# Optimization experiments

Measured on AMD Instinct MI355X. Metric: run time of the kernel, lower is better.

The kernel has to match this reference:

```python
import jax, jax.numpy as jnp
from jax import lax
import numpy as np

B, P, G, C = 16, 6000, 128, 10
PC_MIN = np.array([-54.0, -54.0, -5.0], np.float32)
PC_MAX = np.array([54.0, 54.0, 3.0], np.float32)
CENTER_RADIUS = 1.5
CANDIDATE_TOPK = 5
NUM_HEADS = 6
CLS_W, ALPHA, GAMMA = 2.0, 0.25, 2.0
REG_W, IOU_W = 0.25, 0.25
EPS = 1e-12
INF1, INF2 = 10000.0, 100000.0


def _aabb(boxes):
    # boxes: (N,7) [cx,cy,cz,dx,dy,dz,yaw] -> AABB (min,max) of the 8 rotated corners
    c, d, yaw = boxes[:, :3], boxes[:, 3:6], boxes[:, 6]
    ca, sa = jnp.abs(jnp.cos(yaw)), jnp.abs(jnp.sin(yaw))
    hx = 0.5 * (d[:, 0] * ca + d[:, 1] * sa)
    hy = 0.5 * (d[:, 0] * sa + d[:, 1] * ca)
    h = jnp.stack([hx, hy, 0.5 * d[:, 2]], -1)
    return c - h, c + h


def _iou3d(pred7, gt7):
    # axis-aligned 3D IoU over corner AABBs (reference stand-in for rotated BboxOverlaps3D)
    pmin, pmax = _aabb(pred7)
    gmin, gmax = _aabb(gt7)
    lo = jnp.maximum(pmin[:, None], gmin[None])   # (P,G,3)
    hi = jnp.minimum(pmax[:, None], gmax[None])
    inter = jnp.prod(jnp.maximum(hi - lo, 0.0), -1)
    vp = jnp.prod(pmax - pmin, -1)
    vg = jnp.prod(gmax - gmin, -1)
    return inter / (vp[:, None] + vg[None] - inter + 1e-7)


def _cost_matrix(pred_logits, pred_boxes, gt_boxes, gt_labels):
    # --- focal classification cost ---
    p = jax.nn.sigmoid(pred_logits)                                  # (P,C)
    neg = -jnp.log(1.0 - p + EPS) * (1.0 - ALPHA) * p ** GAMMA
    pos = -jnp.log(p + EPS) * ALPHA * (1.0 - p) ** GAMMA
    cls_cost = (pos - neg)[:, gt_labels] * CLS_W                     # (P,G)

    gt_norm = jnp.concatenate([gt_boxes[:, :3], jnp.log(gt_boxes[:, 3:6]),
                               jnp.sin(gt_boxes[:, 6:7]), jnp.cos(gt_boxes[:, 6:7])], -1)  # (G,8)
    reg_cost = jnp.abs(pred_boxes[:, None, :8] - gt_norm[None]).sum(-1) * REG_W

    # --- IoU cost on denormalized pred boxes ---
    yaw = jnp.arctan2(pred_boxes[:, 6], pred_boxes[:, 7])
    pred7 = jnp.concatenate([pred_boxes[:, :3], jnp.exp(pred_boxes[:, 3:6]), yaw[:, None]], -1)
    ious = _iou3d(pred7, gt_boxes)                                   # (P,G)
    iou_cost = -ious * IOU_W

    # --- in-gt-box / in-center geometric prior ---
    ctr = pred_boxes[:, :3]
    gmin, gmax = _aabb(gt_boxes)
    in_box = jnp.all((ctr[:, None] > gmin[None]) & (ctr[:, None] < gmax[None]), -1)  # (P,G)
    gc, gd = gt_boxes[:, :3], gt_boxes[:, 3:6]
    lo = gc - CENTER_RADIUS * gd
    hi = gc + CENTER_RADIUS * gd
    in_ctr = jnp.all((ctr[:, None] > lo[None]) & (ctr[:, None] < hi[None]), -1)
    valid = jnp.any(in_box, 1) | jnp.any(in_ctr, 1)                  # (P,)
    in_both = in_box & in_ctr

    cost = cls_cost + reg_cost + iou_cost + (~in_both).astype(cls_cost.dtype) * 100.0
    cost = cost + (~valid).astype(cls_cost.dtype)[:, None] * INF1
    return cost, ious, valid


def _assign(pred_logits, pred_boxes, gt_boxes, gt_labels, head_idx):
    cost, ious, valid = _cost_matrix(pred_logits, pred_boxes, gt_boxes, gt_labels)

    # dynamic-k per gt: sum of top-k ious minus head-schedule offset, truncated, min 1
    k = min(CANDIDATE_TOPK, P)
    topk_ious = lax.top_k(ious.T, k)[0]                              # (G,k)
    dyn = jnp.maximum((topk_ious.sum(1) - 0.5 * (NUM_HEADS - head_idx)).astype(jnp.int32), 1)

    # per-gt lowest-cost top-dyn selection via double argsort ranks
    ranks = jnp.argsort(jnp.argsort(cost, axis=0), axis=0)           # (P,G)
    matching = (ranks < dyn[None, :]).astype(cost.dtype)

    # priors matched to >1 gt: keep only the min-cost gt
    prior_mask = matching.sum(1) > 1
    onehot_min = jax.nn.one_hot(jnp.argmin(cost, 1), G, dtype=cost.dtype)
    matching = jnp.where(prior_mask[:, None], onehot_min, matching)

    rows = jnp.arange(P)

    def cond(s):
        i, cst, m = s
        return jnp.any(m.sum(0) == 0) & (i < G + 8)

    def body(s):
        i, cst, m = s
        cst = cst + (m.sum(1) > 0).astype(cst.dtype)[:, None] * INF2
        unmatched = m.sum(0) == 0                                    # (G,)
        pos = jnp.argmin(cst, 0)                                     # (G,) best prior per gt
        m = jnp.where((rows[:, None] == pos[None]) & unmatched[None], 1.0, m)
        over = jnp.any(m.sum(1) > 1)
        oh = jax.nn.one_hot(jnp.argmin(cst, 1), G, dtype=cst.dtype)
        m = jnp.where(over & prior_mask[:, None], oh, m)             # stale mask, as in torch source
        return i + 1, cst, m

    _, _, matching = lax.while_loop(cond, body, (jnp.int32(0), cost, matching))

    fg = matching.sum(1) > 0                                         # (P,) foreground mask
    matched = jnp.where(fg, jnp.argmax(matching, 1), -1).astype(jnp.int32)
    return fg, matched


def setup_inputs():
    key = jax.random.key(0)
    k1, k2, k3, k4, k5, k6, k7, k8 = jax.random.split(key, 8)
    pred_logits = jax.random.normal(k1, (B, P, C), jnp.float32)
    ctr = jax.random.uniform(k2, (B, P, 3), jnp.float32, jnp.array(PC_MIN), jnp.array(PC_MAX))
    logsz = jnp.log(jax.random.uniform(k3, (B, P, 3), jnp.float32, 1.0, 4.0))
    ang = jax.random.uniform(k4, (B, P, 1), jnp.float32, -np.pi, np.pi)
    vel = jax.random.normal(k5, (B, P, 2), jnp.float32)
    pred_boxes = jnp.concatenate([ctr, logsz, jnp.sin(ang), jnp.cos(ang), vel], -1)
    gctr = jax.random.uniform(k6, (B, G, 3), jnp.float32, jnp.array(PC_MIN), jnp.array(PC_MAX))
    gsz = jax.random.uniform(k7, (B, G, 3), jnp.float32, 1.0, 5.0)
    gyaw = jax.random.uniform(k8, (B, G, 1), jnp.float32, -np.pi, np.pi)
    gt_boxes = jnp.concatenate([gctr, gsz, gyaw], -1)
    gt_labels = jax.random.randint(jax.random.fold_in(key, 99), (B, G), 0, C)
    return {"pred_logits": pred_logits, "pred_boxes": pred_boxes,
            "gt_boxes": gt_boxes, "gt_labels": gt_labels, "head_idx": 5}


def reference(pred_logits, pred_boxes, gt_boxes, gt_labels, head_idx):
    f = lambda pl, pb, gb, gl: _assign(pl, pb, gb, gl, head_idx)
    fg, matched = jax.vmap(f)(pred_logits, pred_boxes, gt_boxes, gt_labels)
    return fg, matched
```

## Files before the change

kernel.cpp:

```cpp
#include <hip/hip_runtime.h>
#include <stdint.h>
#include <math.h>

#define NB 16
#define NP 6000
#define NG 128
#define NC 10
#define SELMAX 4
#define GSTR 24
#define CPB 2
#define PS 2
#define PPC 3000
#define QS 12
#define EPIW 128

typedef unsigned long long u64;
#define NBPs ((size_t)NB * NP)

__device__ __forceinline__ uint32_t fkey(float f) {
  uint32_t u = __float_as_uint(f);
  return (u & 0x80000000u) ? ~u : (u | 0x80000000u);
}
__device__ __forceinline__ float fkey_inv(uint32_t k) {
  uint32_t u = (k & 0x80000000u) ? (k & 0x7fffffffu) : ~k;
  return __uint_as_float(u);
}
__device__ __forceinline__ u64 shfl_xor_u64(u64 v, int m) {
  uint32_t lo = (uint32_t)v, hi = (uint32_t)(v >> 32);
  lo = (uint32_t)__shfl_xor((int)lo, m, 64);
  hi = (uint32_t)__shfl_xor((int)hi, m, 64);
  return ((u64)hi << 32) | lo;
}
__device__ __forceinline__ u64 block_min_u64(u64 v, u64* sred, int lane, int wid) {
  for (int o = 1; o < 64; o <<= 1) {
    u64 t = shfl_xor_u64(v, o);
    if (t < v) v = t;
  }
  __syncthreads();
  if (lane == 0) sred[wid] = v;
  __syncthreads();
  u64 r = sred[0];
  if (sred[1] < r) r = sred[1];
  if (sred[2] < r) r = sred[2];
  if (sred[3] < r) r = sred[3];
  return r;
}

__device__ __forceinline__ void ins5max(uint32_t& a0, uint32_t& a1, uint32_t& a2,
                                        uint32_t& a3, uint32_t& a4, uint32_t k) {
  if (k > a4) {
    a4 = k;
    if (a4 > a3) { uint32_t t = a4; a4 = a3; a3 = t; }
    if (a3 > a2) { uint32_t t = a3; a3 = a2; a2 = t; }
    if (a2 > a1) { uint32_t t = a2; a2 = a1; a1 = t; }
    if (a1 > a0) { uint32_t t = a1; a1 = a0; a0 = t; }
  }
}
__device__ __forceinline__ void ins4min(u64& c0, u64& c1, u64& c2, u64& c3, u64 k) {
  if (k < c3) {
    c3 = k;
    if (c3 < c2) { u64 t = c3; c3 = c2; c2 = t; }
    if (c2 < c1) { u64 t = c2; c2 = c1; c1 = t; }
    if (c1 < c0) { u64 t = c1; c1 = c0; c0 = t; }
  }
}
__device__ __forceinline__ void wave_top5_iou(uint32_t a0, uint32_t a1,
                                              uint32_t a2, uint32_t a3,
                                              uint32_t a4, int lane,
                                              float* dst) {
  int hp = 0;
  for (int k = 0; k < 5; ++k) {
    uint32_t cand = (hp == 0) ? a0 : (hp == 1) ? a1 : (hp == 2) ? a2
                  : (hp == 3) ? a3 : (hp == 4) ? a4 : 0u;
    u64 key = ((u64)cand << 32) | (unsigned)lane;
    u64 r = key;
    for (int o = 1; o < 64; o <<= 1) {
      u64 t = shfl_xor_u64(r, o);
      if (t > r) r = t;
    }
    if (lane == 0) dst[k] = fkey_inv((uint32_t)(r >> 32));
    if (r == key) hp++;
  }
}
__device__ __forceinline__ void wave_top4_cost(u64 c0, u64 c1, u64 c2, u64 c3,
                                               int lane, u64* dst) {
  int hp = 0;
  for (int k = 0; k < 4; ++k) {
    u64 cand = (hp == 0) ? c0 : (hp == 1) ? c1 : (hp == 2) ? c2
             : (hp == 3) ? c3 : ~0ull;
    u64 r = cand;
    for (int o = 1; o < 64; o <<= 1) {
      u64 t = shfl_xor_u64(r, o);
      if (t < r) r = t;
    }
    if (lane == 0) dst[k] = r;
    if (r == cand) hp++;
  }
}

__global__ __launch_bounds__(256) void prep_kernel(
    const float* __restrict__ gt_boxes,
    const int* __restrict__ gt_labels,
    const float* __restrict__ pred_logits,
    const float* __restrict__ pred_boxes,
    float* __restrict__ gtaux,
    float* __restrict__ paux,
    float* __restrict__ clst,
    int* __restrict__ rowcnt,
    int* __restrict__ rowassign,
    int* __restrict__ colcnt,
    int* __restrict__ wcount) {
#pragma clang fp contract(off)
  __shared__ float shg[NG * 12];
  const int b = blockIdx.y, tid = threadIdx.x;
  if (tid < NG) {
    const int g = tid;
    const float* gb = gt_boxes + ((size_t)b * NG + g) * 7;
    float cx = gb[0], cy = gb[1], cz = gb[2];
    float dx = gb[3], dy = gb[4], dz = gb[5];
    float yaw = gb[6];
    float cyw = cosf(yaw), syw = sinf(yaw);
    float ca = fabsf(cyw), sa = fabsf(syw);
    float hx = 0.5f * (dx * ca + dy * sa);
    float hy = 0.5f * (dx * sa + dy * ca);
    float hz = 0.5f * dz;
    float gmin0 = cx - hx, gmin1 = cy - hy, gmin2 = cz - hz;
    float gmax0 = cx + hx, gmax1 = cy + hy, gmax2 = cz + hz;
    float* s = &shg[g * 12];
    s[0] = gmin0; s[1] = gmin1; s[2] = gmin2;
    s[3] = gmax0; s[4] = gmax1; s[5] = gmax2;
    s[6] = cx - 1.5f * dx; s[7] = cy - 1.5f * dy; s[8] = cz - 1.5f * dz;
    s[9] = cx + 1.5f * dx; s[10] = cy + 1.5f * dy; s[11] = cz + 1.5f * dz;
    if (blockIdx.x == 0) {
      float vg = ((gmax0 - gmin0) * (gmax1 - gmin1)) * (gmax2 - gmin2);
      float* o = gtaux + ((size_t)b * NG + g) * GSTR;
      o[0] = gmin0; o[1] = gmin1; o[2] = gmin2;
      o[3] = gmax0; o[4] = gmax1; o[5] = gmax2;
      o[6] = s[6]; o[7] = s[7]; o[8] = s[8];
      o[9] = s[9]; o[10] = s[10]; o[11] = s[11];
      o[12] = cx; o[13] = cy; o[14] = cz;
      o[15] = logf(dx); o[16] = logf(dy); o[17] = logf(dz);
      o[18] = syw; o[19] = cyw;
      o[20] = vg;
      o[21] = __int_as_float(gt_labels[(size_t)b * NG + g]);
      o[22] = 0.0f; o[23] = 0.0f;
      colcnt[b * NG + g] = 0;
      if (b == 0 && g == 0) wcount[0] = 0;
    }
  }
  __syncthreads();
  const int p = blockIdx.x * 256 + tid;
  if (p >= NP) return;
  const size_t idx = (size_t)b * NP + p;
  const float* lg = pred_logits + idx * NC;
  for (int c = 0; c < NC; ++c) {
    float x = lg[c];
    float pr = 1.0f / (1.0f + expf(-x));
    float neg = (-logf(1.0f - pr + 1e-12f) * 0.75f) * (pr * pr);
    float pos = (-logf(pr + 1e-12f) * 0.25f) * ((1.0f - pr) * (1.0f - pr));
    clst[(size_t)c * NBPs + idx] = (pos - neg) * 2.0f;
  }
  const float* bx = pred_boxes + idx * 10;
  float b0 = bx[0], b1 = bx[1], b2 = bx[2], b3 = bx[3], b4 = bx[4];
  float b5 = bx[5], b6 = bx[6], b7 = bx[7];
  float yaw = atan2f(b6, b7);
  float d0 = expf(b3), d1 = expf(b4), d2 = expf(b5);
  float ca = fabsf(cosf(yaw)), sa = fabsf(sinf(yaw));
  float hx = 0.5f * (d0 * ca + d1 * sa);
  float hy = 0.5f * (d0 * sa + d1 * ca);
  float hz = 0.5f * d2;
  float pmin0 = b0 - hx, pmin1 = b1 - hy, pmin2 = b2 - hz;
  float pmax0 = b0 + hx, pmax1 = b1 + hy, pmax2 = b2 + hz;
  int valid = 0;
  for (int g = 0; g < NG; ++g) {
    const float* s = &shg[g * 12];
    bool inb = (b0 > s[0]) && (b0 < s[3]) && (b1 > s[1]) && (b1 < s[4]) &&
               (b2 > s[2]) && (b2 < s[5]);
    bool inc = (b0 > s[6]) && (b0 < s[9]) && (b1 > s[7]) && (b1 < s[10]) &&
               (b2 > s[8]) && (b2 < s[11]);
    if (inb || inc) { valid = 1; break; }
  }
  float* o = paux + idx * 16;
  o[0] = b0; o[1] = b1; o[2] = b2; o[3] = b3;
  o[4] = b4; o[5] = b5; o[6] = b6; o[7] = b7;
  o[8] = pmin0; o[9] = pmin1; o[10] = pmin2;
  o[11] = pmax0; o[12] = pmax1; o[13] = pmax2;
  o[14] = ((pmax0 - pmin0) * (pmax1 - pmin1)) * (pmax2 - pmin2);
  o[15] = valid ? 0.0f : 10000.0f;
  rowcnt[idx] = 0;
  rowassign[idx] = 0x7fffffff;
}

struct GTp {
  float gmin0, gmin1, gmin2, gmax0, gmax1, gmax2;
  float lo0, lo1, lo2, hi0, hi1, hi2;
  float gtn0, gtn1, gtn2, gtn3, gtn4, gtn5, gtn6, gtn7;
  float vg;
  int label;
};
__device__ __forceinline__ GTp load_gt(const float* __restrict__ gtaux,
                                       int b, int g) {
  const float* ga = gtaux + ((size_t)b * NG + g) * GSTR;
  GTp t;
  t.gmin0 = ga[0]; t.gmin1 = ga[1]; t.gmin2 = ga[2];
  t.gmax0 = ga[3]; t.gmax1 = ga[4]; t.gmax2 = ga[5];
  t.lo0 = ga[6]; t.lo1 = ga[7]; t.lo2 = ga[8];
  t.hi0 = ga[9]; t.hi1 = ga[10]; t.hi2 = ga[11];
  t.gtn0 = ga[12]; t.gtn1 = ga[13]; t.gtn2 = ga[14]; t.gtn3 = ga[15];
  t.gtn4 = ga[16]; t.gtn5 = ga[17]; t.gtn6 = ga[18]; t.gtn7 = ga[19];
  t.vg = ga[20];
  t.label = __float_as_int(ga[21]);
  return t;
}

__device__ __forceinline__ float cost_base(
    float b0, float b1, float b2, float b3, float b4, float b5, float b6,
    float b7, float pmin0, float pmin1, float pmin2, float pmax0, float pmax1,
    float pmax2, float vp, float cls, const GTp& t, float* iou_out) {
#pragma clang fp contract(off)
  float r = fabsf(b0 - t.gtn0);
  r = r + fabsf(b1 - t.gtn1);
  r = r + fabsf(b2 - t.gtn2);
  r = r + fabsf(b3 - t.gtn3);
  r = r + fabsf(b4 - t.gtn4);
  r = r + fabsf(b5 - t.gtn5);
  r = r + fabsf(b6 - t.gtn6);
  r = r + fabsf(b7 - t.gtn7);
  float reg = r * 0.25f;
  float li0 = fmaxf(pmin0, t.gmin0), li1 = fmaxf(pmin1, t.gmin1),
        li2 = fmaxf(pmin2, t.gmin2);
  float hj0 = fminf(pmax0, t.gmax0), hj1 = fminf(pmax1, t.gmax1),
        hj2 = fminf(pmax2, t.gmax2);
  float e0 = fmaxf(hj0 - li0, 0.0f), e1 = fmaxf(hj1 - li1, 0.0f),
        e2 = fmaxf(hj2 - li2, 0.0f);
  float inter = (e0 * e1) * e2;
  float iou = inter / (((vp + t.vg) - inter) + 1e-7f);
  bool inb = (b0 > t.gmin0) && (b0 < t.gmax0) && (b1 > t.gmin1) &&
             (b1 < t.gmax1) && (b2 > t.gmin2) && (b2 < t.gmax2);
  bool inc = (b0 > t.lo0) && (b0 < t.hi0) && (b1 > t.lo1) && (b1 < t.hi1) &&
             (b2 > t.lo2) && (b2 < t.hi2);
  *iou_out = iou;
  return ((cls + reg) + (-(iou * 0.25f))) + ((inb && inc) ? 0.0f : 100.0f);
}

__device__ __forceinline__ void eval_fast(
    float b0, float b1, float b2, float b3, float b4, float b5, float b6,
    float b7, float pmin0, float pmin1, float pmin2, float pmax0, float pmax1,
    float pmax2, float vp, float cls, const GTp& t,
    uint32_t& a0, uint32_t& a1, uint32_t& a2, uint32_t& a3, uint32_t& a4,
    float* cc_out) {
#pragma clang fp contract(off)
  float r = fabsf(b0 - t.gtn0);
  r = r + fabsf(b1 - t.gtn1);
  r = r + fabsf(b2 - t.gtn2);
  r = r + fabsf(b3 - t.gtn3);
  r = r + fabsf(b4 - t.gtn4);
  r = r + fabsf(b5 - t.gtn5);
  r = r + fabsf(b6 - t.gtn6);
  r = r + fabsf(b7 - t.gtn7);
  float reg = r * 0.25f;
  bool ov = (pmin0 < t.gmax0) && (pmax0 > t.gmin0) &&
            (pmin1 < t.gmax1) && (pmax1 > t.gmin1) &&
            (pmin2 < t.gmax2) && (pmax2 > t.gmin2);
  float cc;
  if (ov) {
    float li0 = fmaxf(pmin0, t.gmin0), li1 = fmaxf(pmin1, t.gmin1),
          li2 = fmaxf(pmin2, t.gmin2);
    float hj0 = fminf(pmax0, t.gmax0), hj1 = fminf(pmax1, t.gmax1),
          hj2 = fminf(pmax2, t.gmax2);
    float e0 = fmaxf(hj0 - li0, 0.0f), e1 = fmaxf(hj1 - li1, 0.0f),
          e2 = fmaxf(hj2 - li2, 0.0f);
    float inter = (e0 * e1) * e2;
    float iou = inter / (((vp + t.vg) - inter) + 1e-7f);
    bool inb = (b0 > t.gmin0) && (b0 < t.gmax0) && (b1 > t.gmin1) &&
               (b1 < t.gmax1) && (b2 > t.gmin2) && (b2 < t.gmax2);
    bool inc = (b0 > t.lo0) && (b0 < t.hi0) && (b1 > t.lo1) && (b1 < t.hi1) &&
               (b2 > t.lo2) && (b2 < t.hi2);
    cc = ((cls + reg) + (-(iou * 0.25f))) + ((inb && inc) ? 0.0f : 100.0f);
    ins5max(a0, a1, a2, a3, a4, fkey(iou));
  } else {
    cc = (cls + reg) + 100.0f;
  }
  *cc_out = cc;
}

__global__ __launch_bounds__(256) void select_kernel(
    const float* __restrict__ paux,
    const float* __restrict__ clst,
    const float* __restrict__ gtaux,
    float* __restrict__ iou5F,
    u64* __restrict__ ckF) {
#pragma clang fp contract(off)
  const int n = blockIdx.x;
  const int orig = (n & 7) * 256 + (n >> 3);
  const int b = orig >> 7;
  const int rem = orig & 127;
  const int gq = rem >> 1, ps = rem & 1;
  const int g0 = gq * CPB;
  const int tid = threadIdx.x;
  const int lane = tid & 63, wid = tid >> 6;

  const GTp t0 = load_gt(gtaux, b, g0);
  const GTp t1 = load_gt(gtaux, b, g0 + 1);
  const size_t rowbase = (size_t)b * NP;
  const int pbase = ps * PPC;

  const uint32_t Z = fkey(0.0f);
  uint32_t i0a = Z, i0b = Z, i0c = Z, i0d = Z, i0e = Z;
  uint32_t i1a = Z, i1b = Z, i1c = Z, i1d = Z, i1e = Z;
  u64 k0a = ~0ull, k0b = ~0ull, k0c = ~0ull, k0d = ~0ull;
  u64 k1a = ~0ull, k1b = ~0ull, k1c = ~0ull, k1d = ~0ull;

  for (int q = 0; q < QS; ++q) {
    const int off = q * 256 + tid;
    if (off < PPC) {
      const int p = pbase + off;
      const size_t idx = rowbase + p;
      const float4* pa = (const float4*)(paux + idx * 16);
      float4 A = pa[0], B = pa[1], C = pa[2], D = pa[3];
      float cls0 = clst[(size_t)t0.label * NBPs + idx];
      float cls1 = clst[(size_t)t1.label * NBPs + idx];
      float cc0, cc1;
      eval_fast(A.x, A.y, A.z, A.w, B.x, B.y, B.z, B.w,
                C.x, C.y, C.z, C.w, D.x, D.y, D.z, cls0, t0,
                i0a, i0b, i0c, i0d, i0e, &cc0);
      eval_fast(A.x, A.y, A.z, A.w, B.x, B.y, B.z, B.w,
                C.x, C.y, C.z, C.w, D.x, D.y, D.z, cls1, t1,
                i1a, i1b, i1c, i1d, i1e, &cc1);
      ins4min(k0a, k0b, k0c, k0d, ((u64)fkey(cc0 + D.w) << 32) | (unsigned)p);
      ins4min(k1a, k1b, k1c, k1d, ((u64)fkey(cc1 + D.w) << 32) | (unsigned)p);
    }
  }

  __shared__ float iouW[4][CPB][5];
  __shared__ u64 ckW[4][CPB][4];
  wave_top5_iou(i0a, i0b, i0c, i0d, i0e, lane, &iouW[wid][0][0]);
  wave_top5_iou(i1a, i1b, i1c, i1d, i1e, lane, &iouW[wid][1][0]);
  wave_top4_cost(k0a, k0b, k0c, k0d, lane, &ckW[wid][0][0]);
  wave_top4_cost(k1a, k1b, k1c, k1d, lane, &ckW[wid][1][0]);
  __syncthreads();

  if (tid < CPB) {
    const int c = tid;
    const int col = b * NG + g0 + c;
    float m0 = -INFINITY, m1 = -INFINITY, m2 = -INFINITY, m3 = -INFINITY,
          m4 = -INFINITY;
    for (int w = 0; w < 4; ++w) {
      for (int j = 0; j < 5; ++j) {
        float v = iouW[w][c][j];
        if (v > m4) {
          m4 = v;
          if (m4 > m3) { float t = m4; m4 = m3; m3 = t; }
          if (m3 > m2) { float t = m3; m3 = m2; m2 = t; }
          if (m2 > m1) { float t = m2; m2 = m1; m1 = t; }
          if (m1 > m0) { float t = m1; m1 = m0; m0 = t; }
        }
      }
    }
    u64 s0 = ~0ull, s1 = ~0ull, s2 = ~0ull, s3 = ~0ull;
    for (int w = 0; w < 4; ++w) {
      for (int j = 0; j < 4; ++j) {
        u64 k = ckW[w][c][j];
        if (k < s3) {
          s3 = k;
          if (s3 < s2) { u64 t = s3; s3 = s2; s2 = t; }
          if (s2 < s1) { u64 t = s2; s2 = s1; s1 = t; }
          if (s1 < s0) { u64 t = s1; s1 = s0; s0 = t; }
        }
      }
    }
    float* fi = iou5F + (size_t)col * (PS * 5) + ps * 5;
    fi[0] = m0; fi[1] = m1; fi[2] = m2; fi[3] = m3; fi[4] = m4;
    u64* fc = ckF + (size_t)col * (PS * 4) + ps * 4;
    fc[0] = s0; fc[1] = s1; fc[2] = s2; fc[3] = s3;
  }
}

__global__ __launch_bounds__(256) void merge_kernel(
    const float* __restrict__ iou5F,
    const u64* __restrict__ ckF,
    const int* __restrict__ head_ptr,
    int* __restrict__ colsel,
    int* __restrict__ rowcnt,
    int* __restrict__ rowassign,
    int* __restrict__ wlist,
    int* __restrict__ wcount) {
#pragma clang fp contract(off)
  const int col = blockIdx.x * 256 + threadIdx.x;
  if (col >= NB * NG) return;
  const int b = col / NG, g = col - b * NG;
  const float* ip = iou5F + (size_t)col * (PS * 5);
  float m0 = -INFINITY, m1 = -INFINITY, m2 = -INFINITY, m3 = -INFINITY,
        m4 = -INFINITY;
  for (int i = 0; i < PS * 5; ++i) {
    float v = ip[i];
    if (v > m4) {
      m4 = v;
      if (m4 > m3) { float t = m4; m4 = m3; m3 = t; }
      if (m3 > m2) { float t = m3; m3 = m2; m2 = t; }
      if (m2 > m1) { float t = m2; m2 = m1; m1 = t; }
      if (m1 > m0) { float t = m1; m1 = m0; m0 = t; }
    }
  }
  float sum5 = ((((m0 + m1) + m2) + m3) + m4);
  float adj = sum5 - 0.5f * (float)(6 - head_ptr[0]);
  int dyn = (int)adj;
  if (dyn < 1) dyn = 1;
  if (dyn > SELMAX) dyn = SELMAX;

  const u64* kp = ckF + (size_t)col * (PS * 4);
  u64 s0 = ~0ull, s1 = ~0ull, s2 = ~0ull, s3 = ~0ull;
  for (int i = 0; i < PS * 4; ++i) {
    u64 k = kp[i];
    if (k < s3) {
      s3 = k;
      if (s3 < s2) { u64 t = s3; s3 = s2; s2 = t; }
      if (s2 < s1) { u64 t = s2; s2 = s1; s1 = t; }
      if (s1 < s0) { u64 t = s1; s1 = s0; s0 = t; }
    }
  }
  const size_t rowbase = (size_t)b * NP;
  int pk[4];
  pk[0] = (int)(s0 & 0xffffffffu);
  pk[1] = (int)(s1 & 0xffffffffu);
  pk[2] = (int)(s2 & 0xffffffffu);
  pk[3] = (int)(s3 & 0xffffffffu);
  for (int k = 0; k < SELMAX; ++k) {
    int sel = (k < dyn) ? pk[k] : -1;
    colsel[(size_t)col * SELMAX + k] = sel;
    if (sel >= 0) {
      int old = atomicAdd(&rowcnt[rowbase + sel], 1);
      if (old == 1) {
        int slot = atomicAdd(wcount, 1);
        wlist[slot] = (int)(rowbase + sel);
      }
      atomicMin(&rowassign[rowbase + sel], g);
    }
  }
}

__global__ __launch_bounds__(256) void epi_kernel(
    const float* __restrict__ paux,
    const float* __restrict__ clst,
    const float* __restrict__ gtaux,
    const int* __restrict__ colsel,
    const int* __restrict__ rowcnt,
    const int* __restrict__ wlist,
    const int* __restrict__ wcount,
    int* __restrict__ rowminArr,
    int* __restrict__ colcnt) {
#pragma clang fp contract(off)
  const int tid = threadIdx.x;
  if (blockIdx.x >= EPIW) {
    const int col = (blockIdx.x - EPIW) * 256 + tid;
    if (col < NB * NG) {
      const int b = col / NG;
      int cnt = 0;
      const size_t cb = (size_t)col * SELMAX;
      for (int k = 0; k < SELMAX; ++k) {
        int s = colsel[cb + k];
        if (s >= 0 && rowcnt[(size_t)b * NP + s] == 1) cnt++;
      }
      if (cnt) atomicAdd(&colcnt[col], cnt);
    }
    return;
  }
  const int lane = tid & 63, wid = tid >> 6;
  const int wavesTotal = EPIW * 4;
  const int wave = blockIdx.x * 4 + wid;
  const int n = wcount[0];
  for (int e = wave; e < n; e += wavesTotal) {
    const int idx = wlist[e];
    const int b = idx / NP;
    const float4* pa = (const float4*)(paux + (size_t)idx * 16);
    float4 A = pa[0], Bq = pa[1], Cq = pa[2], Dq = pa[3];
    const float pen = Dq.w;
    u64 best = ~0ull;
    for (int h = 0; h < 2; ++h) {
      const int g = h * 64 + lane;
      GTp t = load_gt(gtaux, b, g);
      float cls = clst[(size_t)t.label * NBPs + idx];
      float iou;
      float cc = cost_base(A.x, A.y, A.z, A.w, Bq.x, Bq.y, Bq.z, Bq.w,
                           Cq.x, Cq.y, Cq.z, Cq.w, Dq.x, Dq.y, Dq.z,
                           cls, t, &iou);
      u64 key = ((u64)fkey(cc + pen) << 32) | (unsigned)g;
      if (key < best) best = key;
    }
    for (int o = 1; o < 64; o <<= 1) {
      u64 t = shfl_xor_u64(best, o);
      if (t < best) best = t;
    }
    if (lane == 0) {
      const int bg = (int)(best & 0xffffffffu);
      rowminArr[idx] = bg;
      atomicAdd(&colcnt[b * NG + bg], 1);
    }
  }
}

__global__ __launch_bounds__(256) void fixup_kernel(
    const float* __restrict__ paux,
    const float* __restrict__ clst,
    const float* __restrict__ gtaux,
    const int* __restrict__ colcnt,
    const int* __restrict__ rowcnt,
    int* __restrict__ rowassign) {
#pragma clang fp contract(off)
  const int g = blockIdx.x, b = blockIdx.y, tid = threadIdx.x;
  if (colcnt[b * NG + g] != 0) return;
  const int lane = tid & 63, wid = tid >> 6;
  const size_t rowbase = (size_t)b * NP;
  GTp t = load_gt(gtaux, b, g);
  u64 best = ~0ull;
  for (int p = tid; p < NP; p += 256) {
    const size_t idx = rowbase + p;
    if (rowcnt[idx] == 0) {
      const float4* pa = (const float4*)(paux + idx * 16);
      float4 A = pa[0], Bq = pa[1], Cq = pa[2], Dq = pa[3];
      float cls = clst[(size_t)t.label * NBPs + idx];
      float iou;
      float cc = cost_base(A.x, A.y, A.z, A.w, Bq.x, Bq.y, Bq.z, Bq.w,
                           Cq.x, Cq.y, Cq.z, Cq.w, Dq.x, Dq.y, Dq.z,
                           cls, t, &iou);
      u64 key = ((u64)fkey(cc + Dq.w) << 32) | (unsigned)p;
      if (key < best) best = key;
    }
  }
  __shared__ u64 sred[4];
  u64 rr = block_min_u64(best, sred, lane, wid);
  if (tid == 0) {
    int pos = (int)(rr & 0xffffffffu);
    atomicMin(&rowassign[rowbase + pos], g);
  }
}

__global__ void output_kernel(const int* __restrict__ rowcnt,
                              const int* __restrict__ rowassign,
                              const int* __restrict__ rowminArr,
                              int* __restrict__ out) {
  const int i = blockIdx.x * 256 + threadIdx.x;
  if (i >= (int)NBPs) return;
  int rc = rowcnt[i];
  int fg, m;
  if (rc == 0) {
    int ra = rowassign[i];
    if (ra == 0x7fffffff) { fg = 0; m = -1; }
    else { fg = 1; m = ra; }
  } else if (rc == 1) {
    fg = 1; m = rowassign[i];
  } else {
    fg = 1; m = rowminArr[i];
  }
  out[i] = fg;
  out[NBPs + i] = m;
}

extern "C" void kernel_launch(void* const* d_in, const int* in_sizes, int n_in,
                              void* d_out, int out_size, void* d_ws, size_t ws_size,
                              hipStream_t stream) {
  const float* pred_logits = (const float*)d_in[0];
  const float* pred_boxes = (const float*)d_in[1];
  const float* gt_boxes = (const float*)d_in[2];
  const int* gt_labels = (const int*)d_in[3];
  const int* head = (const int*)d_in[4];
  (void)in_sizes; (void)n_in; (void)out_size; (void)ws_size;

  char* w = (char*)d_ws;
  size_t off = 0;
  auto alloc = [&](size_t bytes) -> void* {
    void* p = w + off;
    off += (bytes + 255) & ~(size_t)255;
    return p;
  };
  float* paux = (float*)alloc((size_t)NB * NP * 16 * 4);
  float* clst = (float*)alloc((size_t)NC * NB * NP * 4);
  float* gtaux = (float*)alloc((size_t)NB * NG * GSTR * 4);
  float* iou5F = (float*)alloc((size_t)NB * NG * PS * 5 * 4);
  u64* ckF = (u64*)alloc((size_t)NB * NG * PS * 4 * 8);
  int* colsel = (int*)alloc((size_t)NB * NG * SELMAX * 4);
  int* rowcnt = (int*)alloc((size_t)NB * NP * 4);
  int* rowassign = (int*)alloc((size_t)NB * NP * 4);
  int* rowminArr = (int*)alloc((size_t)NB * NP * 4);
  int* colcnt = (int*)alloc((size_t)NB * NG * 4);
  int* wlist = (int*)alloc((size_t)NB * NP * 4);
  int* wcount = (int*)alloc(256);

  int* out = (int*)d_out;
  dim3 blk(256);
  prep_kernel<<<dim3((NP + 255) / 256, NB), blk, 0, stream>>>(
      gt_boxes, gt_labels, pred_logits, pred_boxes, gtaux, paux, clst,
      rowcnt, rowassign, colcnt, wcount);
  select_kernel<<<dim3(NB * (NG / CPB) * PS), blk, 0, stream>>>(
      paux, clst, gtaux, iou5F, ckF);
  merge_kernel<<<dim3((NB * NG + 255) / 256), blk, 0, stream>>>(
      iou5F, ckF, head, colsel, rowcnt, rowassign, wlist, wcount);
  epi_kernel<<<dim3(EPIW + 8), blk, 0, stream>>>(
      paux, clst, gtaux, colsel, rowcnt, wlist, wcount, rowminArr, colcnt);
  fixup_kernel<<<dim3(NG, NB), blk, 0, stream>>>(
      paux, clst, gtaux, colcnt, rowcnt, rowassign);
  output_kernel<<<dim3(((int)NBPs + 255) / 256), blk, 0, stream>>>(
      rowcnt, rowassign, rowminArr, out);
}
```

Measured before the change: 118.6 us.

## Split prep validity scan across waves and process four GT columns per select block

```diff
diff --git a/kernel.cpp b/kernel.cpp
--- a/kernel.cpp
+++ b/kernel.cpp
@@ -8,10 +8,10 @@
 #define NC 10
 #define SELMAX 4
 #define GSTR 24
-#define CPB 2
-#define PS 2
-#define PPC 3000
-#define QS 12
+#define CPB 4
+#define PS 3
+#define PPC 2000
+#define QS 8
 #define EPIW 128
 
 typedef unsigned long long u64;
@@ -98,7 +98,7 @@
   }
 }
 
-__global__ __launch_bounds__(256) void prep_kernel(
+__global__ __launch_bounds__(512) void prep_kernel(
     const float* __restrict__ gt_boxes,
     const int* __restrict__ gt_labels,
     const float* __restrict__ pred_logits,
@@ -112,7 +112,9 @@
     int* __restrict__ wcount) {
 #pragma clang fp contract(off)
   __shared__ float shg[NG * 12];
+  __shared__ int vfl[8][64];
   const int b = blockIdx.y, tid = threadIdx.x;
+  const int lane = tid & 63, sub = tid >> 6;
   if (tid < NG) {
     const int g = tid;
     const float* gb = gt_boxes + ((size_t)b * NG + g) * 7;
@@ -149,46 +151,56 @@
     }
   }
   __syncthreads();
-  const int p = blockIdx.x * 256 + tid;
+  const int p = blockIdx.x * 64 + lane;
+  const size_t idx = (size_t)b * NP + p;
+  int flag = 0;
+  if (p < NP) {
+    const float* bxp = pred_boxes + idx * 10;
+    float b0 = bxp[0], b1 = bxp[1], b2 = bxp[2];
+    for (int g = sub * 16; g < sub * 16 + 16; ++g) {
+      const float* s = &shg[g * 12];
+      bool inb = (b0 > s[0]) && (b0 < s[3]) && (b1 > s[1]) && (b1 < s[4]) &&
+                 (b2 > s[2]) && (b2 < s[5]);
+      bool inc = (b0 > s[6]) && (b0 < s[9]) && (b1 > s[7]) && (b1 < s[10]) &&
+                 (b2 > s[8]) && (b2 < s[11]);
+      if (inb || inc) { flag = 1; break; }
+    }
+  }
+  vfl[sub][lane] = flag;
+  __syncthreads();
   if (p >= NP) return;
-  const size_t idx = (size_t)b * NP + p;
   const float* lg = pred_logits + idx * NC;
-  for (int c = 0; c < NC; ++c) {
+  for (int c = sub; c < NC; c += 8) {
     float x = lg[c];
     float pr = 1.0f / (1.0f + expf(-x));
     float neg = (-logf(1.0f - pr + 1e-12f) * 0.75f) * (pr * pr);
     float pos = (-logf(pr + 1e-12f) * 0.25f) * ((1.0f - pr) * (1.0f - pr));
     clst[(size_t)c * NBPs + idx] = (pos - neg) * 2.0f;
   }
-  const float* bx = pred_boxes + idx * 10;
-  float b0 = bx[0], b1 = bx[1], b2 = bx[2], b3 = bx[3], b4 = bx[4];
-  float b5 = bx[5], b6 = bx[6], b7 = bx[7];
-  float yaw = atan2f(b6, b7);
-  float d0 = expf(b3), d1 = expf(b4), d2 = expf(b5);
-  float ca = fabsf(cosf(yaw)), sa = fabsf(sinf(yaw));
-  float hx = 0.5f * (d0 * ca + d1 * sa);
-  float hy = 0.5f * (d0 * sa + d1 * ca);
-  float hz = 0.5f * d2;
-  float pmin0 = b0 - hx, pmin1 = b1 - hy, pmin2 = b2 - hz;
-  float pmax0 = b0 + hx, pmax1 = b1 + hy, pmax2 = b2 + hz;
-  int valid = 0;
-  for (int g = 0; g < NG; ++g) {
-    const float* s = &shg[g * 12];
-    bool inb = (b0 > s[0]) && (b0 < s[3]) && (b1 > s[1]) && (b1 < s[4]) &&
-               (b2 > s[2]) && (b2 < s[5]);
-    bool inc = (b0 > s[6]) && (b0 < s[9]) && (b1 > s[7]) && (b1 < s[10]) &&
-               (b2 > s[8]) && (b2 < s[11]);
-    if (inb || inc) { valid = 1; break; }
-  }
-  float* o = paux + idx * 16;
-  o[0] = b0; o[1] = b1; o[2] = b2; o[3] = b3;
-  o[4] = b4; o[5] = b5; o[6] = b6; o[7] = b7;
-  o[8] = pmin0; o[9] = pmin1; o[10] = pmin2;
-  o[11] = pmax0; o[12] = pmax1; o[13] = pmax2;
-  o[14] = ((pmax0 - pmin0) * (pmax1 - pmin1)) * (pmax2 - pmin2);
-  o[15] = valid ? 0.0f : 10000.0f;
-  rowcnt[idx] = 0;
-  rowassign[idx] = 0x7fffffff;
+  if (sub == 0) {
+    int valid = vfl[0][lane] | vfl[1][lane] | vfl[2][lane] | vfl[3][lane] |
+                vfl[4][lane] | vfl[5][lane] | vfl[6][lane] | vfl[7][lane];
+    const float* bxp = pred_boxes + idx * 10;
+    float b0 = bxp[0], b1 = bxp[1], b2 = bxp[2], b3 = bxp[3], b4 = bxp[4];
+    float b5 = bxp[5], b6 = bxp[6], b7 = bxp[7];
+    float yaw = atan2f(b6, b7);
+    float d0 = expf(b3), d1 = expf(b4), d2 = expf(b5);
+    float ca = fabsf(cosf(yaw)), sa = fabsf(sinf(yaw));
+    float hx = 0.5f * (d0 * ca + d1 * sa);
+    float hy = 0.5f * (d0 * sa + d1 * ca);
+    float hz = 0.5f * d2;
+    float pmin0 = b0 - hx, pmin1 = b1 - hy, pmin2 = b2 - hz;
+    float pmax0 = b0 + hx, pmax1 = b1 + hy, pmax2 = b2 + hz;
+    float* o = paux + idx * 16;
+    o[0] = b0; o[1] = b1; o[2] = b2; o[3] = b3;
+    o[4] = b4; o[5] = b5; o[6] = b6; o[7] = b7;
+    o[8] = pmin0; o[9] = pmin1; o[10] = pmin2;
+    o[11] = pmax0; o[12] = pmax1; o[13] = pmax2;
+    o[14] = ((pmax0 - pmin0) * (pmax1 - pmin1)) * (pmax2 - pmin2);
+    o[15] = valid ? 0.0f : 10000.0f;
+    rowcnt[idx] = 0;
+    rowassign[idx] = 0x7fffffff;
+  }
 }
 
 struct GTp {
@@ -243,12 +255,12 @@
   return ((cls + reg) + (-(iou * 0.25f))) + ((inb && inc) ? 0.0f : 100.0f);
 }
 
-__device__ __forceinline__ void eval_fast(
+__device__ __forceinline__ void eval_col(
     float b0, float b1, float b2, float b3, float b4, float b5, float b6,
     float b7, float pmin0, float pmin1, float pmin2, float pmax0, float pmax1,
-    float pmax2, float vp, float cls, const GTp& t,
+    float pmax2, float vp, float pen, float cls, const GTp& t, int p,
     uint32_t& a0, uint32_t& a1, uint32_t& a2, uint32_t& a3, uint32_t& a4,
-    float* cc_out) {
+    u64& c0, u64& c1, u64& c2, u64& c3) {
 #pragma clang fp contract(off)
   float r = fabsf(b0 - t.gtn0);
   r = r + fabsf(b1 - t.gtn1);
@@ -281,7 +293,7 @@
   } else {
     cc = (cls + reg) + 100.0f;
   }
-  *cc_out = cc;
+  ins4min(c0, c1, c2, c3, ((u64)fkey(cc + pen) << 32) | (unsigned)p);
 }
 
 __global__ __launch_bounds__(256) void select_kernel(
@@ -292,24 +304,31 @@
     u64* __restrict__ ckF) {
 #pragma clang fp contract(off)
   const int n = blockIdx.x;
-  const int orig = (n & 7) * 256 + (n >> 3);
-  const int b = orig >> 7;
-  const int rem = orig & 127;
-  const int gq = rem >> 1, ps = rem & 1;
+  const int orig = (n & 7) * 192 + (n >> 3);
+  const int b = orig / 96;
+  const int rem = orig - b * 96;
+  const int gq = rem / PS;
+  const int ps = rem - gq * PS;
   const int g0 = gq * CPB;
   const int tid = threadIdx.x;
   const int lane = tid & 63, wid = tid >> 6;
 
   const GTp t0 = load_gt(gtaux, b, g0);
   const GTp t1 = load_gt(gtaux, b, g0 + 1);
+  const GTp t2 = load_gt(gtaux, b, g0 + 2);
+  const GTp t3 = load_gt(gtaux, b, g0 + 3);
   const size_t rowbase = (size_t)b * NP;
   const int pbase = ps * PPC;
 
   const uint32_t Z = fkey(0.0f);
   uint32_t i0a = Z, i0b = Z, i0c = Z, i0d = Z, i0e = Z;
   uint32_t i1a = Z, i1b = Z, i1c = Z, i1d = Z, i1e = Z;
+  uint32_t i2a = Z, i2b = Z, i2c = Z, i2d = Z, i2e = Z;
+  uint32_t i3a = Z, i3b = Z, i3c = Z, i3d = Z, i3e = Z;
   u64 k0a = ~0ull, k0b = ~0ull, k0c = ~0ull, k0d = ~0ull;
   u64 k1a = ~0ull, k1b = ~0ull, k1c = ~0ull, k1d = ~0ull;
+  u64 k2a = ~0ull, k2b = ~0ull, k2c = ~0ull, k2d = ~0ull;
+  u64 k3a = ~0ull, k3b = ~0ull, k3c = ~0ull, k3d = ~0ull;
 
   for (int q = 0; q < QS; ++q) {
     const int off = q * 256 + tid;
@@ -320,15 +339,20 @@
       float4 A = pa[0], B = pa[1], C = pa[2], D = pa[3];
       float cls0 = clst[(size_t)t0.label * NBPs + idx];
       float cls1 = clst[(size_t)t1.label * NBPs + idx];
-      float cc0, cc1;
-      eval_fast(A.x, A.y, A.z, A.w, B.x, B.y, B.z, B.w,
-                C.x, C.y, C.z, C.w, D.x, D.y, D.z, cls0, t0,
-                i0a, i0b, i0c, i0d, i0e, &cc0);
-      eval_fast(A.x, A.y, A.z, A.w, B.x, B.y, B.z, B.w,
-                C.x, C.y, C.z, C.w, D.x, D.y, D.z, cls1, t1,
-                i1a, i1b, i1c, i1d, i1e, &cc1);
-      ins4min(k0a, k0b, k0c, k0d, ((u64)fkey(cc0 + D.w) << 32) | (unsigned)p);
-      ins4min(k1a, k1b, k1c, k1d, ((u64)fkey(cc1 + D.w) << 32) | (unsigned)p);
+      float cls2 = clst[(size_t)t2.label * NBPs + idx];
+      float cls3 = clst[(size_t)t3.label * NBPs + idx];
+      eval_col(A.x, A.y, A.z, A.w, B.x, B.y, B.z, B.w,
+               C.x, C.y, C.z, C.w, D.x, D.y, D.z, D.w, cls0, t0, p,
+               i0a, i0b, i0c, i0d, i0e, k0a, k0b, k0c, k0d);
+      eval_col(A.x, A.y, A.z, A.w, B.x, B.y, B.z, B.w,
+               C.x, C.y, C.z, C.w, D.x, D.y, D.z, D.w, cls1, t1, p,
+               i1a, i1b, i1c, i1d, i1e, k1a, k1b, k1c, k1d);
+      eval_col(A.x, A.y, A.z, A.w, B.x, B.y, B.z, B.w,
+               C.x, C.y, C.z, C.w, D.x, D.y, D.z, D.w, cls2, t2, p,
+               i2a, i2b, i2c, i2d, i2e, k2a, k2b, k2c, k2d);
+      eval_col(A.x, A.y, A.z, A.w, B.x, B.y, B.z, B.w,
+               C.x, C.y, C.z, C.w, D.x, D.y, D.z, D.w, cls3, t3, p,
+               i3a, i3b, i3c, i3d, i3e, k3a, k3b, k3c, k3d);
     }
   }
 
@@ -336,8 +360,12 @@
   __shared__ u64 ckW[4][CPB][4];
   wave_top5_iou(i0a, i0b, i0c, i0d, i0e, lane, &iouW[wid][0][0]);
   wave_top5_iou(i1a, i1b, i1c, i1d, i1e, lane, &iouW[wid][1][0]);
+  wave_top5_iou(i2a, i2b, i2c, i2d, i2e, lane, &iouW[wid][2][0]);
+  wave_top5_iou(i3a, i3b, i3c, i3d, i3e, lane, &iouW[wid][3][0]);
   wave_top4_cost(k0a, k0b, k0c, k0d, lane, &ckW[wid][0][0]);
   wave_top4_cost(k1a, k1b, k1c, k1d, lane, &ckW[wid][1][0]);
+  wave_top4_cost(k2a, k2b, k2c, k2d, lane, &ckW[wid][2][0]);
+  wave_top4_cost(k3a, k3b, k3c, k3d, lane, &ckW[wid][3][0]);
   __syncthreads();
 
   if (tid < CPB) {
@@ -588,7 +616,7 @@
 
   int* out = (int*)d_out;
   dim3 blk(256);
-  prep_kernel<<<dim3((NP + 255) / 256, NB), blk, 0, stream>>>(
+  prep_kernel<<<dim3((NP + 63) / 64, NB), dim3(512), 0, stream>>>(
       gt_boxes, gt_labels, pred_logits, pred_boxes, gtaux, paux, clst,
       rowcnt, rowassign, colcnt, wcount);
   select_kernel<<<dim3(NB * (NG / CPB) * PS), blk, 0, stream>>>(
```

After: 120.1 us. No clear change (+1.2%).
